# Optimization experiments

Measured on AMD Instinct MI355X. Metric: run time of the kernel, lower is better.

Reference implementation:

```python
import jax, jax.numpy as jnp
import numpy as np

N_FEATURES = 512
FEATURE_DIM = 768
HIDDEN_DIM = 256


def setup_inputs() -> dict:
    key = jax.random.key(0)
    k0, k1, k2 = jax.random.split(key, 3)
    feature_embeddings = jax.random.normal(k0, (N_FEATURES, FEATURE_DIM), dtype=jnp.float32)
    # Linear(feature_dim*2 -> hidden) params, PyTorch-style init scale
    W1 = jax.random.normal(k1, (2 * FEATURE_DIM, HIDDEN_DIM), dtype=jnp.float32) / np.sqrt(2 * FEATURE_DIM)
    b1 = jnp.zeros((HIDDEN_DIM,), dtype=jnp.float32)
    W2 = jax.random.normal(k2, (HIDDEN_DIM, 1), dtype=jnp.float32) / np.sqrt(HIDDEN_DIM)
    b2 = jnp.zeros((1,), dtype=jnp.float32)
    return {"feature_embeddings": feature_embeddings, "W1": W1, "b1": b1, "W2": W2, "b2": b2}


def reference(feature_embeddings, W1, b1, W2, b2):
    n = feature_embeddings.shape[0]
    # all (i, j) with i < j -- same order as the original nested loop
    i_idx, j_idx = jnp.triu_indices(n, k=1)          # [P], [P]
    pairs = jnp.concatenate(
        [feature_embeddings[i_idx], feature_embeddings[j_idx]], axis=-1
    )                                                 # [P, 2*feature_dim]
    h = jax.nn.relu(pairs @ W1 + b1)                  # [P, hidden]
    scores = h @ W2 + b2                              # [P, 1]
    return i_idx, j_idx, scores
```

## Files before the change

kernel.cpp:

```cpp
#include <hip/hip_runtime.h>

#define FD 768
#define HD 256
#define NF 512
#define NC 512
#define PAIRS (NF * (NF - 1) / 2)

typedef __attribute__((ext_vector_type(4))) float f32x4;
typedef __attribute__((ext_vector_type(8))) short bf16x8;

__device__ inline unsigned bf16pk(float a, float b) {
    unsigned ua = __float_as_uint(a), ub = __float_as_uint(b);
    ua = (ua + 0x7FFFu + ((ua >> 16) & 1u)) >> 16;
    ub = (ub + 0x7FFFu + ((ub >> 16) & 1u)) >> 16;
    return ua | (ub << 16);
}

__global__ __launch_bounds__(256) void gemm_mfma_kernel(
    const float* __restrict__ E, const float* __restrict__ W1,
    const float* __restrict__ b1, float* __restrict__ C)
{
    __shared__ char lds[2 * 32 * 512];
    char* EtB = lds;
    char* WtB = lds + 32 * 512;

    const int tid  = threadIdx.x;
    const int r0   = blockIdx.y * 32, c0 = blockIdx.x * 32;
    const int c0w  = c0 & 255;
    const int dofs = (c0 >= 256) ? FD : 0;
    const int lane = tid & 63, wave = tid >> 6;
    const int wr = wave >> 1, wc = wave & 1;
    const int m = lane & 15, g = lane >> 4;
    const int arow = 16 * wc + m;
    const int brow = 16 * wr + m;

    f32x4 acc = {0.f, 0.f, 0.f, 0.f};
    const float4* E4 = (const float4*)E;

    for (int rnd = 0; rnd < 3; ++rnd) {
        if (rnd) __syncthreads();

        #pragma unroll
        for (int s = 0; s < 8; ++s) {
            int idx = tid + s * 256;
            int r = idx >> 6, c4 = idx & 63;
            float4 v = E4[(size_t)(r0 + r) * 192 + rnd * 64 + c4];
            uint2 pk;
            pk.x = bf16pk(v.x, v.y);
            pk.y = bf16pk(v.z, v.w);
            int gi = (c4 >> 1) ^ (r & 7);
            *(uint2*)(EtB + r * 512 + gi * 16 + (c4 & 1) * 8) = pk;
        }
        {
            int c = tid & 31, dp = tid >> 5;
            #pragma unroll
            for (int it = 0; it < 16; ++it) {
                int kp = dp + 8 * it;
                int d = dofs + rnd * 256 + 2 * kp;
                float w0 = W1[(size_t)d * 256 + c0w + c];
                float w1 = W1[(size_t)(d + 1) * 256 + c0w + c];
                unsigned pk = bf16pk(w0, w1);
                int gi = (kp >> 2) ^ (c & 7);
                *(unsigned*)(WtB + c * 512 + gi * 16 + (kp & 3) * 4) = pk;
            }
        }
        __syncthreads();

        #pragma unroll
        for (int ks = 0; ks < 8; ++ks) {
            int giA = (4 * ks + g) ^ (arow & 7);
            int giB = (4 * ks + g) ^ (brow & 7);
            bf16x8 af = *(const bf16x8*)(WtB + arow * 512 + giA * 16);
            bf16x8 bf = *(const bf16x8*)(EtB + brow * 512 + giB * 16);
            acc = __builtin_amdgcn_mfma_f32_16x16x32_bf16(af, bf, acc, 0, 0, 0);
        }
    }

    const int row = r0 + 16 * wr + m;
    const int col = c0 + 16 * wc + 4 * g;
    float4 b = {0.f, 0.f, 0.f, 0.f};
    if (c0 < 256) b = ((const float4*)b1)[col >> 2];
    float4 o = {acc[0] + b.x, acc[1] + b.y, acc[2] + b.z, acc[3] + b.w};
    *(float4*)&C[(size_t)row * NC + col] = o;
}

__global__ __launch_bounds__(256) void pair_kernel(
    const float* __restrict__ C, const float* __restrict__ W2,
    const float* __restrict__ b2, float* __restrict__ out)
{
    __shared__ float4 As[16 * 64];
    __shared__ float4 Bs[32 * 64];

    int rem = blockIdx.x, bi = 0;
    while (rem >= 16 - (bi >> 1)) { rem -= 16 - (bi >> 1); ++bi; }
    const int bj = (bi >> 1) + rem;
    const int i0 = bi * 16, j0 = bj * 32;

    const int tid = threadIdx.x;
    const float4* C4 = (const float4*)C;

    #pragma unroll
    for (int s = 0; s < 4; ++s) {
        int idx = tid + 256 * s;
        int row = idx >> 6, c4 = idx & 63;
        As[row * 64 + (c4 ^ ((row >> 1) & 7))] = C4[(i0 + row) * 128 + c4];
    }
    #pragma unroll
    for (int s = 0; s < 8; ++s) {
        int idx = tid + 256 * s;
        int row = idx >> 6, c4 = idx & 63;
        Bs[row * 64 + (c4 ^ ((row >> 1) & 7))] = C4[(j0 + row) * 128 + 64 + c4];
    }
    __syncthreads();

    const int tx = tid & 15, ty = tid >> 4;
    const int keyA = (ty >> 1) & 7, keyB = tx & 7;
    const float4* W24 = (const float4*)W2;

    float acc0 = 0.f, acc1 = 0.f;
    #pragma unroll 8
    for (int k4 = 0; k4 < HD / 4; ++k4) {
        float4 a  = As[ty * 64 + (k4 ^ keyA)];
        float4 b0 = Bs[(2 * tx + 0) * 64 + (k4 ^ keyB)];
        float4 b1v = Bs[(2 * tx + 1) * 64 + (k4 ^ keyB)];
        float4 w = W24[k4];
        acc0 = fmaf(fmaxf(a.x + b0.x, 0.f), w.x, acc0);
        acc0 = fmaf(fmaxf(a.y + b0.y, 0.f), w.y, acc0);
        acc0 = fmaf(fmaxf(a.z + b0.z, 0.f), w.z, acc0);
        acc0 = fmaf(fmaxf(a.w + b0.w, 0.f), w.w, acc0);
        acc1 = fmaf(fmaxf(a.x + b1v.x, 0.f), w.x, acc1);
        acc1 = fmaf(fmaxf(a.y + b1v.y, 0.f), w.y, acc1);
        acc1 = fmaf(fmaxf(a.z + b1v.z, 0.f), w.z, acc1);
        acc1 = fmaf(fmaxf(a.w + b1v.w, 0.f), w.w, acc1);
    }

    const float bias2 = b2[0];
    const int i = i0 + ty;
    #pragma unroll
    for (int u = 0; u < 2; ++u) {
        int j = j0 + 2 * tx + u;
        float v = u ? acc1 : acc0;
        if (j > i) {
            int p = i * (2 * NF - i - 1) / 2 + (j - i - 1);
            out[p]             = (float)i;
            out[PAIRS + p]     = (float)j;
            out[2 * PAIRS + p] = v + bias2;
        }
    }
}

extern "C" void kernel_launch(void* const* d_in, const int* in_sizes, int n_in,
                              void* d_out, int out_size, void* d_ws, size_t ws_size,
                              hipStream_t stream) {
    const float* E  = (const float*)d_in[0];
    const float* W1 = (const float*)d_in[1];
    const float* b1 = (const float*)d_in[2];
    const float* W2 = (const float*)d_in[3];
    const float* b2 = (const float*)d_in[4];
    float* out = (float*)d_out;
    float* C   = (float*)d_ws;

    gemm_mfma_kernel<<<dim3(16, 16), 256, 0, stream>>>(E, W1, b1, C);
    pair_kernel<<<272, 256, 0, stream>>>(C, W2, b2, out);
}
```

Baseline: 27.49 us.

## Pre-convert E and W1 to bf16 in a prep kernel, load MFMA operands directly

Adds a prep kernel that converts the embeddings to bf16 and writes W1 transposed as bf16 into workspace. The GEMM then drops its LDS staging and barriers and loads MFMA fragments straight from global memory. The aim is to stop every GEMM block from redoing the fp32-to-bf16 conversion and the strided W1 gathers. The cost is an extra kernel launch plus a workspace round trip, and uncoalesced 16-byte-per-lane global fragment loads.

```diff
diff --git a/kernel.cpp b/kernel.cpp
--- a/kernel.cpp
+++ b/kernel.cpp
@@ -16,67 +16,55 @@
     return ua | (ub << 16);
 }
 
+__global__ __launch_bounds__(256) void prep_kernel(
+    const float* __restrict__ E, const float* __restrict__ W1,
+    ushort* __restrict__ Ebf, ushort* __restrict__ Wt)
+{
+    const int bid = blockIdx.x, tid = threadIdx.x;
+    if (bid < 384) {
+        int idx = bid * 256 + tid;
+        float4 v = ((const float4*)E)[idx];
+        uint2 pk;
+        pk.x = bf16pk(v.x, v.y);
+        pk.y = bf16pk(v.z, v.w);
+        *(uint2*)(Ebf + (size_t)idx * 4) = pk;
+    } else {
+        int t = (bid - 384) * 256 + tid;
+        int q = t & 127, kp = t >> 7;
+        int off = (q < 64) ? 0 : FD;
+        int cq = q & 63;
+        const float4* W14 = (const float4*)W1;
+        float4 w0 = W14[(size_t)(2 * kp + off) * 64 + cq];
+        float4 w1 = W14[(size_t)(2 * kp + 1 + off) * 64 + cq];
+        *(unsigned*)(Wt + (size_t)(4 * q + 0) * FD + 2 * kp) = bf16pk(w0.x, w1.x);
+        *(unsigned*)(Wt + (size_t)(4 * q + 1) * FD + 2 * kp) = bf16pk(w0.y, w1.y);
+        *(unsigned*)(Wt + (size_t)(4 * q + 2) * FD + 2 * kp) = bf16pk(w0.z, w1.z);
+        *(unsigned*)(Wt + (size_t)(4 * q + 3) * FD + 2 * kp) = bf16pk(w0.w, w1.w);
+    }
+}
+
 __global__ __launch_bounds__(256) void gemm_mfma_kernel(
-    const float* __restrict__ E, const float* __restrict__ W1,
+    const ushort* __restrict__ Ebf, const ushort* __restrict__ Wt,
     const float* __restrict__ b1, float* __restrict__ C)
 {
-    __shared__ char lds[2 * 32 * 512];
-    char* EtB = lds;
-    char* WtB = lds + 32 * 512;
-
     const int tid  = threadIdx.x;
-    const int r0   = blockIdx.y * 32, c0 = blockIdx.x * 32;
-    const int c0w  = c0 & 255;
-    const int dofs = (c0 >= 256) ? FD : 0;
     const int lane = tid & 63, wave = tid >> 6;
     const int wr = wave >> 1, wc = wave & 1;
-    const int m = lane & 15, g = lane >> 4;
-    const int arow = 16 * wc + m;
-    const int brow = 16 * wr + m;
+    const int r0 = blockIdx.y * 32, c0 = blockIdx.x * 32;
+    const int n = lane & 15, g = lane >> 4;
+
+    const ushort* aptr = Wt  + (size_t)(c0 + 16 * wc + n) * FD + 8 * g;
+    const ushort* bptr = Ebf + (size_t)(r0 + 16 * wr + n) * FD + 8 * g;
 
     f32x4 acc = {0.f, 0.f, 0.f, 0.f};
-    const float4* E4 = (const float4*)E;
-
-    for (int rnd = 0; rnd < 3; ++rnd) {
-        if (rnd) __syncthreads();
-
-        #pragma unroll
-        for (int s = 0; s < 8; ++s) {
-            int idx = tid + s * 256;
-            int r = idx >> 6, c4 = idx & 63;
-            float4 v = E4[(size_t)(r0 + r) * 192 + rnd * 64 + c4];
-            uint2 pk;
-            pk.x = bf16pk(v.x, v.y);
-            pk.y = bf16pk(v.z, v.w);
-            int gi = (c4 >> 1) ^ (r & 7);
-            *(uint2*)(EtB + r * 512 + gi * 16 + (c4 & 1) * 8) = pk;
-        }
-        {
-            int c = tid & 31, dp = tid >> 5;
-            #pragma unroll
-            for (int it = 0; it < 16; ++it) {
-                int kp = dp + 8 * it;
-                int d = dofs + rnd * 256 + 2 * kp;
-                float w0 = W1[(size_t)d * 256 + c0w + c];
-                float w1 = W1[(size_t)(d + 1) * 256 + c0w + c];
-                unsigned pk = bf16pk(w0, w1);
-                int gi = (kp >> 2) ^ (c & 7);
-                *(unsigned*)(WtB + c * 512 + gi * 16 + (kp & 3) * 4) = pk;
-            }
-        }
-        __syncthreads();
-
-        #pragma unroll
-        for (int ks = 0; ks < 8; ++ks) {
-            int giA = (4 * ks + g) ^ (arow & 7);
-            int giB = (4 * ks + g) ^ (brow & 7);
-            bf16x8 af = *(const bf16x8*)(WtB + arow * 512 + giA * 16);
-            bf16x8 bf = *(const bf16x8*)(EtB + brow * 512 + giB * 16);
-            acc = __builtin_amdgcn_mfma_f32_16x16x32_bf16(af, bf, acc, 0, 0, 0);
-        }
+    #pragma unroll 8
+    for (int ks = 0; ks < 24; ++ks) {
+        bf16x8 af = *(const bf16x8*)(aptr + 32 * ks);
+        bf16x8 bf = *(const bf16x8*)(bptr + 32 * ks);
+        acc = __builtin_amdgcn_mfma_f32_16x16x32_bf16(af, bf, acc, 0, 0, 0);
     }
 
-    const int row = r0 + 16 * wr + m;
+    const int row = r0 + 16 * wr + n;
     const int col = c0 + 16 * wc + 4 * g;
     float4 b = {0.f, 0.f, 0.f, 0.f};
     if (c0 < 256) b = ((const float4*)b1)[col >> 2];
@@ -120,8 +108,8 @@
     float acc0 = 0.f, acc1 = 0.f;
     #pragma unroll 8
     for (int k4 = 0; k4 < HD / 4; ++k4) {
-        float4 a  = As[ty * 64 + (k4 ^ keyA)];
-        float4 b0 = Bs[(2 * tx + 0) * 64 + (k4 ^ keyB)];
+        float4 a   = As[ty * 64 + (k4 ^ keyA)];
+        float4 b0  = Bs[(2 * tx + 0) * 64 + (k4 ^ keyB)];
         float4 b1v = Bs[(2 * tx + 1) * 64 + (k4 ^ keyB)];
         float4 w = W24[k4];
         acc0 = fmaf(fmaxf(a.x + b0.x, 0.f), w.x, acc0);
@@ -158,8 +146,12 @@
     const float* W2 = (const float*)d_in[3];
     const float* b2 = (const float*)d_in[4];
     float* out = (float*)d_out;
-    float* C   = (float*)d_ws;
 
-    gemm_mfma_kernel<<<dim3(16, 16), 256, 0, stream>>>(E, W1, b1, C);
+    ushort* Ebf = (ushort*)d_ws;
+    ushort* Wt  = Ebf + (size_t)NF * FD;
+    float*  C   = (float*)((char*)d_ws + 2 * (size_t)NF * FD * 2);
+
+    prep_kernel<<<576, 256, 0, stream>>>(E, W1, Ebf, Wt);
+    gemm_mfma_kernel<<<dim3(16, 16), 256, 0, stream>>>(Ebf, Wt, b1, C);
     pair_kernel<<<272, 256, 0, stream>>>(C, W2, b2, out);
 }
```

New measurement: 28.20 us. 1.03x slower.
